# Optimization experiments

Hardware: AMD Instinct MI355X
Metric: run time of the kernel (lower is better)

## Reference

```python
import jax, jax.numpy as jnp
import numpy as np

STRIDES = (8, 16, 32)
IMG = 1024
CENTER_RADIUS = 2.5
N_CAND = 10  # SimOTA candidate top-k


def setup_inputs() -> dict:
    key = jax.random.key(0)
    ks = jax.random.split(key, 6)
    B, G = 16, 100
    sizes = [IMG // s for s in STRIDES]
    inp = {}
    for i, H in enumerate(sizes):
        inp[f"reg{i}"] = jax.random.normal(ks[i], (B, 4, H, H), jnp.float32)
        inp[f"obj{i}"] = jax.random.normal(ks[3 + i], (B, 1, H, H), jnp.float32)
    rng = np.random.default_rng(0)
    cxy = rng.uniform(64.0, IMG - 64.0, (B, G, 2))
    wh = rng.uniform(16.0, 160.0, (B, G, 2))
    labels = np.concatenate([np.zeros((B, G, 1)), cxy, wh], axis=-1).astype(np.float32)
    counts = rng.integers(20, G + 1, B)  # variable num_gt per image, zero-padded tail
    mask = (np.arange(G)[None, :] < counts[:, None]).astype(np.float32)
    labels = labels * mask[:, :, None]
    inp["labels"] = jnp.asarray(labels)
    return inp


def _decode(regs, objs):
    outs, xs, ys, ss = [], [], [], []
    for reg, obj, s in zip(regs, objs, STRIDES):
        B, _, H, W = reg.shape
        o = jnp.concatenate([reg, obj], axis=1).transpose(0, 2, 3, 1).reshape(B, H * W, 5)
        yv, xv = jnp.meshgrid(jnp.arange(H), jnp.arange(W), indexing="ij")
        grid = jnp.stack([xv, yv], axis=-1).reshape(-1, 2).astype(o.dtype)  # [HW,2] (x,y)
        xy = (o[..., :2] + grid) * s
        wh = jnp.exp(o[..., 2:4]) * s
        outs.append(jnp.concatenate([xy, wh, o[..., 4:5]], axis=-1))
        xs.append(grid[:, 0])
        ys.append(grid[:, 1])
        ss.append(jnp.full((H * W,), float(s), o.dtype))
    return (jnp.concatenate(outs, 1), jnp.concatenate(xs), jnp.concatenate(ys), jnp.concatenate(ss))


def _pairwise_iou(gt, pr):
    # gt [G,4], pr [A,4] in cxcywh -> [G,A]
    tl = jnp.maximum(gt[:, None, :2] - gt[:, None, 2:] * 0.5, pr[None, :, :2] - pr[None, :, 2:] * 0.5)
    br = jnp.minimum(gt[:, None, :2] + gt[:, None, 2:] * 0.5, pr[None, :, :2] + pr[None, :, 2:] * 0.5)
    en = jnp.all(tl < br, axis=-1)
    area_i = jnp.prod(br - tl, axis=-1) * en
    area_g = gt[:, 2] * gt[:, 3]
    area_p = pr[:, 2] * pr[:, 3]
    return area_i / (area_g[:, None] + area_p[None, :] - area_i + 1e-16)


def _iou_loss(pred, tgt):
    # elementwise cxcywh IoU loss: 1 - iou**2 (loss_type='iou')
    tl = jnp.maximum(pred[..., :2] - pred[..., 2:] * 0.5, tgt[..., :2] - tgt[..., 2:] * 0.5)
    br = jnp.minimum(pred[..., :2] + pred[..., 2:] * 0.5, tgt[..., :2] + tgt[..., 2:] * 0.5)
    en = jnp.all(tl < br, axis=-1)
    area_i = jnp.prod(br - tl, axis=-1) * en
    area_p = pred[..., 2] * pred[..., 3]
    area_g = tgt[..., 2] * tgt[..., 3]
    iou = area_i / (area_p + area_g - area_i + 1e-16)
    return 1.0 - iou ** 2


def _assign(gt_boxes, gt_valid, bbox, obj_logit, x_c, y_c, strides):
    # SimOTA assignment for one image. gt_boxes [G,4], bbox [A,4].
    G = gt_boxes.shape[0]
    gx, gy, gw, gh = gt_boxes[:, 0], gt_boxes[:, 1], gt_boxes[:, 2], gt_boxes[:, 3]
    bl = x_c[None] - (gx - 0.5 * gw)[:, None]
    br_ = (gx + 0.5 * gw)[:, None] - x_c[None]
    bt = y_c[None] - (gy - 0.5 * gh)[:, None]
    bb = (gy + 0.5 * gh)[:, None] - y_c[None]
    in_boxes = jnp.minimum(jnp.minimum(bl, br_), jnp.minimum(bt, bb)) > 0
    r = CENTER_RADIUS * strides[None]
    cl = x_c[None] - (gx[:, None] - r)
    cr = (gx[:, None] + r) - x_c[None]
    ct = y_c[None] - (gy[:, None] - r)
    cb = (gy[:, None] + r) - y_c[None]
    in_centers = jnp.minimum(jnp.minimum(cl, cr), jnp.minimum(ct, cb)) > 0
    fg_anchor = jnp.any(in_boxes, 0) | jnp.any(in_centers, 0)
    in_both = in_boxes & in_centers

    ious = _pairwise_iou(gt_boxes, bbox)                       # [G,A]
    valid_pair = gt_valid[:, None] & fg_anchor[None, :]
    ious_m = jnp.where(valid_pair, ious, 0.0)
    obj_cost = jax.nn.softplus(-obj_logit)[None, :]            # BCE-with-logits, target=1
    cost = (obj_cost + 3.0 * (-jnp.log(ious + 1e-8))
            + 1e5 * (~in_both) + 1e7 * (~valid_pair))

    topk_ious = jax.lax.top_k(ious_m, N_CAND)[0]               # [G,10]
    dyn_k = jnp.maximum(topk_ious.sum(1).astype(jnp.int32), 1)  # dynamic k per gt
    ranks = jnp.argsort(jnp.argsort(cost, axis=1), axis=1)      # rank of each anchor per gt
    matching = (ranks < dyn_k[:, None]) & gt_valid[:, None]
    n_match = matching.sum(0)
    best_gt = jnp.argmin(cost, axis=0)                          # conflict resolution
    resolved = (jnp.arange(G)[:, None] == best_gt[None, :]) & gt_valid[:, None]
    matching = jnp.where(n_match[None, :] > 1, resolved, matching)
    fg = jnp.any(matching, 0)
    matched_gt = jnp.argmax(matching, 0)
    return fg, matched_gt, fg.sum()


def reference(reg0, reg1, reg2, obj0, obj1, obj2, labels):
    out, x_sh, y_sh, strides = _decode((reg0, reg1, reg2), (obj0, obj1, obj2))
    bbox = out[..., :4]          # [B,A,4] decoded cxcywh
    obj_logit = out[..., 4]      # [B,A]
    x_c = (x_sh + 0.5) * strides
    y_c = (y_sh + 0.5) * strides
    gt_boxes = labels[..., 1:5]
    gt_valid = labels.sum(-1) > 0
    fg, matched_gt, nfg = jax.vmap(_assign, in_axes=(0, 0, 0, 0, None, None, None))(
        gt_boxes, gt_valid, bbox, obj_logit, x_c, y_c, strides)
    num_fg = jnp.maximum(nfg.sum().astype(jnp.float32), 1.0)
    reg_tgt = jax.vmap(lambda g, i: g[i])(gt_boxes, matched_gt)  # [B,A,4]
    fgf = fg.astype(jnp.float32)
    loss_iou = (_iou_loss(bbox, reg_tgt) * fgf).sum() / num_fg
    bce = jax.nn.softplus(obj_logit) - obj_logit * fgf           # BCEWithLogits
    loss_obj = bce.sum() / num_fg
    num_gts = jnp.maximum(gt_valid.sum().astype(jnp.float32), 1.0)
    loss = 5.0 * loss_iou + loss_obj
    return (loss, 5.0 * loss_iou, loss_obj, jnp.float32(0.0), num_fg / num_gts)
```

## Files before the change

### kernel.cpp

```cpp
#include <hip/hip_runtime.h>
#include <math.h>

#define NA   21504
#define NA0  16384
#define NA01 20480
#define NG   100
#define NB   16
#define NC   10
#define NCHK 84
#define NBLK 1344
#define MAXC 192
#define MCAP 1024
#define MSTRIDE 64
#define NSQ  4

__device__ __forceinline__ float softplusf(float x) {
    return fmaxf(x, 0.f) + log1pf(expf(-fabsf(x)));
}

__device__ __forceinline__ unsigned int fmono(float f) {
    unsigned int u = __float_as_uint(f);
    return (f < 0.f) ? ~u : (u | 0x80000000u);
}

__global__ __launch_bounds__(256) void k_decode(
    const float* __restrict__ reg0, const float* __restrict__ obj0,
    const float* __restrict__ reg1, const float* __restrict__ obj1,
    const float* __restrict__ reg2, const float* __restrict__ obj2,
    const float* __restrict__ labels,
    float4* __restrict__ A0, float* __restrict__ OC,
    int* __restrict__ cidx, int* __restrict__ bcnt,
    float* __restrict__ pSp)
{
    int b  = blockIdx.y;
    int bx = blockIdx.x;
    int tid = threadIdx.x;
    int a = bx * 256 + tid;

    int W, ry0, rows; float s;
    if (bx < 64)      { W = 128; s = 8.f;  ry0 = bx * 2;        rows = 2; }
    else if (bx < 80) { W = 64;  s = 16.f; ry0 = (bx - 64) * 4; rows = 4; }
    else              { W = 32;  s = 32.f; ry0 = (bx - 80) * 8; rows = 8; }

    __shared__ unsigned int smask[8];
    if (tid < 8) smask[tid] = 0u;
    __syncthreads();

    if (tid < NG) {
        const float* L = labels + (b * NG + tid) * 5;
        float gx = L[1], gy = L[2], gw = L[3], gh = L[4];
        float r = 2.5f * s;
        float tlx = gx - 0.5f * gw, tly = gy - 0.5f * gh;
        float brx = gx + 0.5f * gw, bry = gy + 0.5f * gh;
        float cxl = gx - r, cxh = gx + r, cyl = gy - r, cyh = gy + r;
        float lox = fminf(tlx, cxl), hix = fmaxf(brx, cxh);
        float loy = fminf(tly, cyl), hiy = fmaxf(bry, cyh);
        int ixA = (int)floorf(lox / s - 0.5f) - 1;
        int ixB = (int)ceilf (hix / s - 0.5f) + 1;
        int iyA = (int)floorf(loy / s - 0.5f) - 1;
        int iyB = (int)ceilf (hiy / s - 0.5f) + 1;
        ixA = max(ixA, 0); ixB = min(ixB, W - 1);
        iyA = max(iyA, ry0); iyB = min(iyB, ry0 + rows - 1);
        for (int iy = iyA; iy <= iyB; iy++) {
            float yc = ((float)iy + 0.5f) * s;
            float mb = fminf(yc - tly, bry - yc);
            float mc = fminf(yc - cyl, cyh - yc);
            for (int ix = ixA; ix <= ixB; ix++) {
                float xc = ((float)ix + 0.5f) * s;
                bool inb = fminf(fminf(xc - tlx, brx - xc), mb) > 0.f;
                bool inc = fminf(fminf(xc - cxl, cxh - xc), mc) > 0.f;
                if (inb || inc) {
                    int bit = (iy - ry0) * W + ix;
                    atomicOr(&smask[bit >> 5], 1u << (bit & 31));
                }
            }
        }
    }

    int x, y, hw, loc;
    const float* regp; const float* objp;
    if (a < NA0)       { x = a & 127;           y = a >> 7; hw = 16384; loc = y * 128 + x; regp = reg0; objp = obj0; }
    else if (a < NA01) { int i = a - NA0;  x = i & 63; y = i >> 6; hw = 4096;  loc = y * 64 + x;  regp = reg1; objp = obj1; }
    else               { int i = a - NA01; x = i & 31; y = i >> 5; hw = 1024;  loc = y * 32 + x;  regp = reg2; objp = obj2; }

    float r0 = regp[(b * 4 + 0) * hw + loc];
    float r1 = regp[(b * 4 + 1) * hw + loc];
    float r2 = regp[(b * 4 + 2) * hw + loc];
    float r3 = regp[(b * 4 + 3) * hw + loc];
    float ol = objp[b * hw + loc];

    float px = (r0 + (float)x) * s, py = (r1 + (float)y) * s;
    float pw = expf(r2) * s,        ph = expf(r3) * s;
    float ocv = softplusf(-ol);

    __syncthreads();
    bool fga = (smask[tid >> 5] >> (tid & 31)) & 1u;

    int idx = b * NA + a;
    if (fga) {
        A0[idx] = make_float4(px - 0.5f * pw, py - 0.5f * ph, px + 0.5f * pw, py + 0.5f * ph);
        OC[idx] = ocv;
    }

    float sp = ocv + ol;
    for (int off = 32; off > 0; off >>= 1) sp += __shfl_down(sp, off);

    unsigned long long mask = __ballot(fga);
    int lane = tid & 63, wid = tid >> 6;
    __shared__ float wSp[4];
    __shared__ int   wcnt[4];
    if (lane == 0) { wSp[wid] = sp; wcnt[wid] = __popcll(mask); }
    __syncthreads();
    int wbase = 0;
    #pragma unroll
    for (int w2 = 0; w2 < 4; w2++) if (w2 < wid) wbase += wcnt[w2];
    if (fga) {
        int prefix = __popcll(mask & ((1ull << lane) - 1ull));
        cidx[b * NA + bx * 256 + wbase + prefix] = a;
    }
    if (tid == 0) {
        bcnt[b * NCHK + bx] = wcnt[0] + wcnt[1] + wcnt[2] + wcnt[3];
        pSp[b * NCHK + bx]  = wSp[0] + wSp[1] + wSp[2] + wSp[3];
    }
}

__global__ __launch_bounds__(256) void k_pack(
    const float4* __restrict__ A0, const float* __restrict__ OC,
    const int* __restrict__ cidx, const int* __restrict__ bcnt,
    float4* __restrict__ PK0, float* __restrict__ PKO, int* __restrict__ PKA,
    int* __restrict__ fcnt,
    int* __restrict__ n_match, int* __restrict__ mg_min,
    unsigned long long* __restrict__ bestkey,
    int* __restrict__ mcount, int* __restrict__ fbflag)
{
    int b = blockIdx.y, bx = blockIdx.x, tid = threadIdx.x;
    int v = 0;
    for (int i = tid; i < bx; i += 256) v += bcnt[b * NCHK + i];
    for (int off = 32; off > 0; off >>= 1) v += __shfl_down(v, off);
    __shared__ int ws[4];
    int wid = tid >> 6;
    if ((tid & 63) == 0) ws[wid] = v;
    __syncthreads();
    int base = ws[0] + ws[1] + ws[2] + ws[3];
    int nt = bcnt[b * NCHK + bx];
    if (tid < nt) {
        int a = cidx[b * NA + bx * 256 + tid];
        int idx = b * NA + a;
        int d = b * NA + base + tid;
        PK0[d] = A0[idx];
        PKO[d] = OC[idx];
        PKA[d] = a;
        n_match[idx] = 0;
        mg_min[idx]  = 0x7fffffff;
        bestkey[idx] = 0xFFFFFFFFFFFFFFFFull;
    }
    if (bx == NCHK - 1 && tid == 0) fcnt[b] = base + nt;
    if (bx == 0 && tid == 0) { mcount[b * MSTRIDE] = 0; fbflag[b] = 0; }
}

__global__ __launch_bounds__(256) void k_assign(
    const float* __restrict__ labels, const float4* __restrict__ A0,
    const float* __restrict__ OC,
    const float4* __restrict__ PK0, const float* __restrict__ PKO,
    const int* __restrict__ PKA, const int* __restrict__ fcnt,
    int* __restrict__ n_match, int* __restrict__ mg_min,
    int* __restrict__ mlist, int* __restrict__ mcount,
    unsigned long long* __restrict__ bestkey, int* __restrict__ fbflag)
{
    int blk = blockIdx.x;
    int b = blk / NG, g = blk % NG;
    const float* L = labels + (b * NG + g) * 5;
    float l0 = L[0], gx = L[1], gy = L[2], gw = L[3], gh = L[4];
    bool gv = (l0 + gx + gy + gw + gh) > 0.f;
    if (!gv) return;
    int tid = threadIdx.x;

    float g_tlx = gx - 0.5f * gw, g_tly = gy - 0.5f * gh;
    float g_brx = gx + 0.5f * gw, g_bry = gy + 0.5f * gh;
    float ag = gw * gh;
    int bbase = b * NA;

    __shared__ float sio[256 * NC];
    __shared__ int   si2[256 * NC];
    __shared__ int   cand_a[MAXC];
    __shared__ float cand_c[MAXC];
    __shared__ int   scnt;
    if (tid == 0) scnt = 0;
    __syncthreads();

    int cnt = fcnt[b];

    float tio[NC];
    #pragma unroll
    for (int k = 0; k < NC; k++) tio[k] = 0.f;

    for (int m = tid; m < cnt; m += 256) {
        float4 c0 = PK0[bbase + m];
        float tlx = fmaxf(g_tlx, c0.x), tly = fmaxf(g_tly, c0.y);
        float brx = fminf(g_brx, c0.z), bry = fminf(g_bry, c0.w);
        if (tlx < brx && tly < bry) {
            float ai = (brx - tlx) * (bry - tly);
            float pa = (c0.z - c0.x) * (c0.w - c0.y);
            float iou = ai / (ag + pa - ai + 1e-16f);
            if (iou > tio[NC - 1]) {
                tio[NC - 1] = iou;
                #pragma unroll
                for (int j = NC - 1; j > 0; --j) {
                    if (tio[j] > tio[j - 1]) { float t = tio[j]; tio[j] = tio[j - 1]; tio[j - 1] = t; }
                }
            }
        }
    }

    #pragma unroll
    for (int k = 0; k < NC; k++) sio[tid * NC + k] = tio[k];
    __syncthreads();

    for (int off = 128; off > 0; off >>= 1) {
        if (tid < off) {
            int abase = tid * NC, bb2 = (tid + off) * NC;
            int i = 0, j = 0;
            float oo_[NC];
            #pragma unroll
            for (int k = 0; k < NC; k++) {
                float va = sio[abase + i], vb = sio[bb2 + j];
                bool ta = va >= vb;
                oo_[k] = ta ? va : vb;
                i += ta ? 1 : 0; j += ta ? 0 : 1;
            }
            #pragma unroll
            for (int k = 0; k < NC; k++) sio[abase + k] = oo_[k];
        }
        __syncthreads();
    }

    float s10 = 0.f;
    #pragma unroll
    for (int k = 0; k < NC; k++) s10 += sio[k];
    int dk = (int)s10;
    if (dk < 1) dk = 1;
    if (dk > NC) dk = NC;

    for (int lev = 0; lev < 3; lev++) {
        float s  = (lev == 0) ? 8.f : ((lev == 1) ? 16.f : 32.f);
        int   W  = (lev == 0) ? 128 : ((lev == 1) ? 64 : 32);
        int aofs = (lev == 0) ? 0 : ((lev == 1) ? NA0 : NA01);
        float rr = 2.5f * s;
        float gxr_lo = gx - rr, gxr_hi = gx + rr;
        float gyr_lo = gy - rr, gyr_hi = gy + rr;
        float lox = fmaxf(g_tlx, gxr_lo), hix = fminf(g_brx, gxr_hi);
        float loy = fmaxf(g_tly, gyr_lo), hiy = fminf(g_bry, gyr_hi);
        int ixA = (int)floorf(lox / s - 0.5f) - 1;
        int ixB = (int)ceilf (hix / s - 0.5f) + 1;
        int iyA = (int)floorf(loy / s - 0.5f) - 1;
        int iyB = (int)ceilf (hiy / s - 0.5f) + 1;
        ixA = max(ixA, 0); ixB = min(ixB, W - 1);
        iyA = max(iyA, 0); iyB = min(iyB, W - 1);
        int nx = ixB - ixA + 1, ny = iyB - iyA + 1;
        int nt = (nx > 0 && ny > 0) ? nx * ny : 0;
        for (int t = tid; t < nt; t += 256) {
            int ix = ixA + t % nx, iy = iyA + t / nx;
            float xcA = ((float)ix + 0.5f) * s;
            float ycA = ((float)iy + 0.5f) * s;
            float bl = xcA - g_tlx, brr = g_brx - xcA;
            float bt = ycA - g_tly, bbb = g_bry - ycA;
            bool inb = fminf(fminf(bl, brr), fminf(bt, bbb)) > 0.f;
            float cl = xcA - gxr_lo, cr = gxr_hi - xcA;
            float ct = ycA - gyr_lo, cb = gyr_hi - ycA;
            bool inc = fminf(fminf(cl, cr), fminf(ct, cb)) > 0.f;
            if (inb && inc) {
                int p = atomicAdd(&scnt, 1);
                if (p < MAXC) cand_a[p] = aofs + iy * W + ix;
            }
        }
    }
    __syncthreads();
    int nc_ = min(scnt, MAXC);

    if (dk <= nc_) {
        for (int ci = tid; ci < nc_; ci += 256) {
            int a = cand_a[ci];
            float4 c0 = A0[bbase + a];
            float pa = (c0.z - c0.x) * (c0.w - c0.y);
            float tlx = fmaxf(g_tlx, c0.x), tly = fmaxf(g_tly, c0.y);
            float brx = fminf(g_brx, c0.z), bry = fminf(g_bry, c0.w);
            bool en = (tlx < brx) && (tly < bry);
            float ai = en ? (brx - tlx) * (bry - tly) : 0.f;
            float iou = ai / (ag + pa - ai + 1e-16f);
            float c = OC[bbase + a] + 3.0f * (-__logf(iou + 1e-8f));
            cand_c[ci] = c;
            unsigned long long key = ((unsigned long long)fmono(c) << 32) | (unsigned int)g;
            atomicMin(&bestkey[bbase + a], key);
        }
        __syncthreads();
        for (int ci = tid; ci < nc_; ci += 256) {
            float c = cand_c[ci]; int a = cand_a[ci];
            int rank = 0;
            for (int j = 0; j < nc_; j++) {
                float cj = cand_c[j]; int aj = cand_a[j];
                rank += (cj < c || (cj == c && aj < a)) ? 1 : 0;
            }
            if (rank < dk) {
                if (atomicAdd(&n_match[bbase + a], 1) == 0) {
                    int p = atomicAdd(&mcount[b * MSTRIDE], 1);
                    mlist[b * MCAP + p] = a;
                }
                atomicMin(&mg_min[bbase + a], g);
            }
        }
    } else {
        if (tid == 0) fbflag[b] = 1;
        float fc[NC]; int fa[NC];
        #pragma unroll
        for (int k = 0; k < NC; k++) { fc[k] = 3.4e38f; fa[k] = 0x7fffffff; }
        for (int m = tid; m < cnt; m += 256) {
            int a = PKA[bbase + m];
            float4 c0 = PK0[bbase + m];
            float pa = (c0.z - c0.x) * (c0.w - c0.y);
            float tlx = fmaxf(g_tlx, c0.x), tly = fmaxf(g_tly, c0.y);
            float brx = fminf(g_brx, c0.z), bry = fminf(g_bry, c0.w);
            bool en = (tlx < brx) && (tly < bry);
            float ai = en ? (brx - tlx) * (bry - tly) : 0.f;
            float iou = ai / (ag + pa - ai + 1e-16f);
            int xx, yy; float s2;
            if (a < NA0)       { xx = a & 127;           yy = a >> 7;  s2 = 8.f;  }
            else if (a < NA01) { int i2 = a - NA0;  xx = i2 & 63; yy = i2 >> 6; s2 = 16.f; }
            else               { int i2 = a - NA01; xx = i2 & 31; yy = i2 >> 5; s2 = 32.f; }
            float xcA = ((float)xx + 0.5f) * s2, ycA = ((float)yy + 0.5f) * s2;
            float rr2 = 2.5f * s2;
            float bl = xcA - g_tlx, brr = g_brx - xcA;
            float bt = ycA - g_tly, bbb = g_bry - ycA;
            bool inb = fminf(fminf(bl, brr), fminf(bt, bbb)) > 0.f;
            float cl = xcA - (gx - rr2), cr = (gx + rr2) - xcA;
            float ct = ycA - (gy - rr2), cb = (gy + rr2) - ycA;
            bool inc = fminf(fminf(cl, cr), fminf(ct, cb)) > 0.f;
            float c = PKO[bbase + m] + 3.0f * (-__logf(iou + 1e-8f));
            if (!(inb && inc)) c += 100000.0f;
            if (c < fc[NC - 1] || (c == fc[NC - 1] && a < fa[NC - 1])) {
                fc[NC - 1] = c; fa[NC - 1] = a;
                #pragma unroll
                for (int j = NC - 1; j > 0; --j) {
                    bool sw = (fc[j] < fc[j - 1]) || (fc[j] == fc[j - 1] && fa[j] < fa[j - 1]);
                    if (sw) {
                        float t1 = fc[j]; fc[j] = fc[j - 1]; fc[j - 1] = t1;
                        int   t2 = fa[j]; fa[j] = fa[j - 1]; fa[j - 1] = t2;
                    }
                }
            }
        }
        __syncthreads();
        #pragma unroll
        for (int k = 0; k < NC; k++) { sio[tid * NC + k] = fc[k]; si2[tid * NC + k] = fa[k]; }
        __syncthreads();
        for (int off = 128; off > 0; off >>= 1) {
            if (tid < off) {
                int abase = tid * NC, bb2 = (tid + off) * NC;
                int i = 0, j = 0;
                float oc_[NC]; int oi_[NC];
                #pragma unroll
                for (int k = 0; k < NC; k++) {
                    float ca = sio[abase + i], cb3 = sio[bb2 + j];
                    int   ia = si2[abase + i], ib  = si2[bb2 + j];
                    bool ta = (ca < cb3) || (ca == cb3 && ia <= ib);
                    oc_[k] = ta ? ca : cb3; oi_[k] = ta ? ia : ib;
                    i += ta ? 1 : 0; j += ta ? 0 : 1;
                }
                #pragma unroll
                for (int k = 0; k < NC; k++) { sio[abase + k] = oc_[k]; si2[abase + k] = oi_[k]; }
            }
            __syncthreads();
        }
        if (tid == 0) {
            for (int k = 0; k < dk; k++) {
                int aa = si2[k];
                if (aa != 0x7fffffff) {
                    if (atomicAdd(&n_match[bbase + aa], 1) == 0) {
                        int p = atomicAdd(&mcount[b * MSTRIDE], 1);
                        mlist[b * MCAP + p] = aa;
                    }
                    atomicMin(&mg_min[bbase + aa], g);
                }
            }
        }
    }
}

__global__ __launch_bounds__(256) void k_sparse(
    const float* __restrict__ labels,
    const float* __restrict__ obj0, const float* __restrict__ obj1,
    const float* __restrict__ obj2,
    const float4* __restrict__ A0, const float* __restrict__ OC,
    const int* __restrict__ n_match, const int* __restrict__ mg_min,
    const int* __restrict__ mlist, const int* __restrict__ mcount,
    const unsigned long long* __restrict__ bestkey, const int* __restrict__ fbflag,
    float* __restrict__ pIl2, float* __restrict__ pOl, int* __restrict__ pNf2)
{
    int q = blockIdx.x;
    int b = blockIdx.y;
    int tid = threadIdx.x;
    __shared__ float lbl[NG * 5];
    for (int i = tid; i < NG * 5; i += 256) lbl[i] = labels[b * NG * 5 + i];
    __syncthreads();

    int cm = min(mcount[b * MSTRIDE], MCAP);
    int fb = fbflag[b];
    float il_s = 0.f, ol_s = 0.f; int nf = 0;

    for (int m = q * 256 + tid; m < cm; m += NSQ * 256) {
        int a = mlist[b * MCAP + m];
        int idx = b * NA + a;
        int n = n_match[idx];

        int x, y, hw, loc; const float* objp; float s, rr;
        if (a < NA0)       { x = a & 127;            y = a >> 7;  hw = 16384; loc = y * 128 + x; objp = obj0; s = 8.f;  rr = 20.f; }
        else if (a < NA01) { int i2 = a - NA0;  x = i2 & 63; y = i2 >> 6; hw = 4096; loc = y * 64 + x; objp = obj1; s = 16.f; rr = 40.f; }
        else               { int i2 = a - NA01; x = i2 & 31; y = i2 >> 5; hw = 1024; loc = y * 32 + x; objp = obj2; s = 32.f; rr = 80.f; }

        float4 c0 = A0[idx];
        bool fg = false; int mg = 0;
        if (n == 1) { fg = true; mg = mg_min[idx]; }
        else {
            unsigned long long key = fb ? 0xFFFFFFFFFFFFFFFFull : bestkey[idx];
            if (key != 0xFFFFFFFFFFFFFFFFull) {
                fg = true; mg = (int)(key & 0xFFFFFFFFull);
            } else {
                float pa = (c0.z - c0.x) * (c0.w - c0.y);
                float oc = OC[idx];
                float xcA = ((float)x + 0.5f) * s, ycA = ((float)y + 0.5f) * s;
                float bestc = 3.4e38f; int bg = 0;
                for (int g = 0; g < NG; g++) {
                    float l0 = lbl[g * 5 + 0], gx = lbl[g * 5 + 1], gy = lbl[g * 5 + 2];
                    float gw = lbl[g * 5 + 3], gh = lbl[g * 5 + 4];
                    bool gvv = (l0 + gx + gy + gw + gh) > 0.f;
                    float tlx = fmaxf(gx - 0.5f * gw, c0.x), tly = fmaxf(gy - 0.5f * gh, c0.y);
                    float brx = fminf(gx + 0.5f * gw, c0.z), bry = fminf(gy + 0.5f * gh, c0.w);
                    bool en = (tlx < brx) && (tly < bry);
                    float ai = en ? (brx - tlx) * (bry - tly) : 0.f;
                    float iou = ai / (gw * gh + pa - ai + 1e-16f);
                    float bl = xcA - (gx - 0.5f * gw), br = (gx + 0.5f * gw) - xcA;
                    float bt = ycA - (gy - 0.5f * gh), bb = (gy + 0.5f * gh) - ycA;
                    bool inb = fminf(fminf(bl, br), fminf(bt, bb)) > 0.f;
                    float cl = xcA - (gx - rr), cr = (gx + rr) - xcA;
                    float ct = ycA - (gy - rr), cb = (gy + rr) - ycA;
                    bool inc = fminf(fminf(cl, cr), fminf(ct, cb)) > 0.f;
                    float c = oc + 3.0f * (-__logf(iou + 1e-8f));
                    if (!(inb && inc)) c += 100000.0f;
                    if (!gvv)          c += 10000000.0f;
                    if (c < bestc) { bestc = c; bg = g; }
                }
                bool gvv = (lbl[bg * 5 + 0] + lbl[bg * 5 + 1] + lbl[bg * 5 + 2] +
                            lbl[bg * 5 + 3] + lbl[bg * 5 + 4]) > 0.f;
                if (gvv) { fg = true; mg = bg; }
            }
        }

        if (fg) {
            float pa = (c0.z - c0.x) * (c0.w - c0.y);
            float gx = lbl[mg * 5 + 1], gy = lbl[mg * 5 + 2];
            float gw = lbl[mg * 5 + 3], gh = lbl[mg * 5 + 4];
            float tlx = fmaxf(c0.x, gx - 0.5f * gw);
            float tly = fmaxf(c0.y, gy - 0.5f * gh);
            float brx = fminf(c0.z, gx + 0.5f * gw);
            float bry = fminf(c0.w, gy + 0.5f * gh);
            bool en = (tlx < brx) && (tly < bry);
            float ai = en ? (brx - tlx) * (bry - tly) : 0.f;
            float iou = ai / (pa + gw * gh - ai + 1e-16f);
            il_s += 1.f - iou * iou;
            ol_s += objp[b * hw + loc];
            nf++;
        }
    }

    for (int off = 32; off > 0; off >>= 1) {
        il_s += __shfl_down(il_s, off);
        ol_s += __shfl_down(ol_s, off);
        nf   += __shfl_down(nf, off);
    }
    __shared__ float wI[4], wO[4];
    __shared__ int   wN[4];
    int wid = tid >> 6;
    if ((tid & 63) == 0) { wI[wid] = il_s; wO[wid] = ol_s; wN[wid] = nf; }
    __syncthreads();
    if (tid == 0) {
        int pb = b * NSQ + q;
        pIl2[pb] = wI[0] + wI[1] + wI[2] + wI[3];
        pOl[pb]  = wO[0] + wO[1] + wO[2] + wO[3];
        pNf2[pb] = wN[0] + wN[1] + wN[2] + wN[3];
    }
}

__global__ __launch_bounds__(256) void k_fin(
    const float* __restrict__ pSp, const float* __restrict__ pIl2,
    const float* __restrict__ pOl, const int* __restrict__ pNf2,
    const float* __restrict__ labels, float* __restrict__ out)
{
    int tid = threadIdx.x;
    double dSp = 0.0;
    for (int i = tid; i < NBLK; i += 256) dSp += (double)pSp[i];
    double dIl = 0.0, dOl = 0.0; int nf = 0;
    for (int i = tid; i < NB * NSQ; i += 256) {
        dIl += (double)pIl2[i];
        dOl += (double)pOl[i];
        nf  += pNf2[i];
    }
    int ng = 0;
    for (int i = tid; i < NB * NG; i += 256) {
        const float* L = labels + i * 5;
        if (L[0] + L[1] + L[2] + L[3] + L[4] > 0.f) ng++;
    }
    for (int off = 32; off > 0; off >>= 1) {
        dSp += __shfl_down(dSp, off);
        dIl += __shfl_down(dIl, off);
        dOl += __shfl_down(dOl, off);
        nf  += __shfl_down(nf, off);
        ng  += __shfl_down(ng, off);
    }
    __shared__ double sSp[4], sIl[4], sOl[4];
    __shared__ int sNf[4], sNg[4];
    int wid = tid >> 6;
    if ((tid & 63) == 0) { sSp[wid] = dSp; sIl[wid] = dIl; sOl[wid] = dOl; sNf[wid] = nf; sNg[wid] = ng; }
    __syncthreads();
    if (tid == 0) {
        double tSp = sSp[0] + sSp[1] + sSp[2] + sSp[3];
        double tIl = sIl[0] + sIl[1] + sIl[2] + sIl[3];
        double tOl = sOl[0] + sOl[1] + sOl[2] + sOl[3];
        int tNf = sNf[0] + sNf[1] + sNf[2] + sNf[3];
        int tNg = sNg[0] + sNg[1] + sNg[2] + sNg[3];
        float num_fg  = fmaxf((float)tNf, 1.f);
        float num_gts = fmaxf((float)tNg, 1.f);
        float li = (float)(tIl / (double)num_fg);
        float lo = (float)((tSp - tOl) / (double)num_fg);
        out[0] = 5.f * li + lo;
        out[1] = 5.f * li;
        out[2] = lo;
        out[3] = 0.f;
        out[4] = num_fg / num_gts;
    }
}

extern "C" void kernel_launch(void* const* d_in, const int* in_sizes, int n_in,
                              void* d_out, int out_size, void* d_ws, size_t ws_size,
                              hipStream_t stream)
{
    const float* reg0   = (const float*)d_in[0];
    const float* obj0   = (const float*)d_in[1];
    const float* reg1   = (const float*)d_in[2];
    const float* obj1   = (const float*)d_in[3];
    const float* reg2   = (const float*)d_in[4];
    const float* obj2   = (const float*)d_in[5];
    const float* labels = (const float*)d_in[6];
    float* out = (float*)d_out;

    char* w = (char*)d_ws;
    size_t off = 0;
    int*    mcount = (int*)(w + off);     off += (size_t)NB * MSTRIDE * 4;
    int*    bcnt   = (int*)(w + off);     off += (size_t)NB * NCHK * 4;
    int*    fcnt   = (int*)(w + off);     off += (size_t)NB * 4;
    int*    fbflag = (int*)(w + off);     off += (size_t)NB * 4;
    float*  pSp    = (float*)(w + off);   off += (size_t)NBLK * 4;
    float*  pIl2   = (float*)(w + off);   off += (size_t)NB * NSQ * 4;
    float*  pOl    = (float*)(w + off);   off += (size_t)NB * NSQ * 4;
    int*    pNf2   = (int*)(w + off);     off += (size_t)NB * NSQ * 4;
    off = (off + 255) & ~(size_t)255;
    float4* A0      = (float4*)(w + off); off += (size_t)NB * NA * 16;
    float4* PK0     = (float4*)(w + off); off += (size_t)NB * NA * 16;
    unsigned long long* bestkey = (unsigned long long*)(w + off); off += (size_t)NB * NA * 8;
    float*  OC      = (float*)(w + off);  off += (size_t)NB * NA * 4;
    float*  PKO     = (float*)(w + off);  off += (size_t)NB * NA * 4;
    int*    PKA     = (int*)(w + off);    off += (size_t)NB * NA * 4;
    int*    cidx    = (int*)(w + off);    off += (size_t)NB * NA * 4;
    int*    n_match = (int*)(w + off);    off += (size_t)NB * NA * 4;
    int*    mg_min  = (int*)(w + off);    off += (size_t)NB * NA * 4;
    int*    mlist   = (int*)(w + off);    off += (size_t)NB * MCAP * 4;

    dim3 gA(NCHK, NB);

    k_decode<<<gA, 256, 0, stream>>>(reg0, obj0, reg1, obj1, reg2, obj2, labels,
                                     A0, OC, cidx, bcnt, pSp);
    k_pack<<<gA, 256, 0, stream>>>(A0, OC, cidx, bcnt, PK0, PKO, PKA, fcnt,
                                   n_match, mg_min, bestkey, mcount, fbflag);
    k_assign<<<dim3(NB * NG), 256, 0, stream>>>(labels, A0, OC, PK0, PKO, PKA, fcnt,
                                                n_match, mg_min, mlist, mcount,
                                                bestkey, fbflag);
    k_sparse<<<dim3(NSQ, NB), 256, 0, stream>>>(labels, obj0, obj1, obj2, A0, OC,
                                                n_match, mg_min, mlist, mcount,
                                                bestkey, fbflag, pIl2, pOl, pNf2);
    k_fin<<<1, 256, 0, stream>>>(pSp, pIl2, pOl, pNf2, labels, out);
}
```

Measured before the change: 122.0 us.

## Fuse pack into decode via atomic compaction and finalize in last sparse block

Result: no change. 123.4 us (+1.2%).

```diff
diff --git a/kernel.cpp b/kernel.cpp
--- a/kernel.cpp
+++ b/kernel.cpp
@@ -11,7 +11,7 @@
 #define NBLK 1344
 #define MAXC 192
 #define MCAP 1024
-#define MSTRIDE 64
+#define CSTRIDE 64
 #define NSQ  4
 
 __device__ __forceinline__ float softplusf(float x) {
@@ -29,7 +29,10 @@
     const float* __restrict__ reg2, const float* __restrict__ obj2,
     const float* __restrict__ labels,
     float4* __restrict__ A0, float* __restrict__ OC,
-    int* __restrict__ cidx, int* __restrict__ bcnt,
+    float4* __restrict__ PK0, float* __restrict__ PKO, int* __restrict__ PKA,
+    int* __restrict__ fcnt,
+    int* __restrict__ n_match, int* __restrict__ mg_min,
+    unsigned long long* __restrict__ bestkey,
     float* __restrict__ pSp)
 {
     int b  = blockIdx.y;
@@ -43,6 +46,9 @@
     else              { W = 32;  s = 32.f; ry0 = (bx - 80) * 8; rows = 8; }
 
     __shared__ unsigned int smask[8];
+    __shared__ float wSp[4];
+    __shared__ int   wcnt[4];
+    __shared__ int   sbase;
     if (tid < 8) smask[tid] = 0u;
     __syncthreads();
 
@@ -95,67 +101,41 @@
 
     __syncthreads();
     bool fga = (smask[tid >> 5] >> (tid & 31)) & 1u;
+    float4 corners = make_float4(px - 0.5f * pw, py - 0.5f * ph,
+                                 px + 0.5f * pw, py + 0.5f * ph);
 
     int idx = b * NA + a;
     if (fga) {
-        A0[idx] = make_float4(px - 0.5f * pw, py - 0.5f * ph, px + 0.5f * pw, py + 0.5f * ph);
+        A0[idx] = corners;
         OC[idx] = ocv;
-    }
-
-    float sp = ocv + ol;
-    for (int off = 32; off > 0; off >>= 1) sp += __shfl_down(sp, off);
-
-    unsigned long long mask = __ballot(fga);
-    int lane = tid & 63, wid = tid >> 6;
-    __shared__ float wSp[4];
-    __shared__ int   wcnt[4];
-    if (lane == 0) { wSp[wid] = sp; wcnt[wid] = __popcll(mask); }
-    __syncthreads();
-    int wbase = 0;
-    #pragma unroll
-    for (int w2 = 0; w2 < 4; w2++) if (w2 < wid) wbase += wcnt[w2];
-    if (fga) {
-        int prefix = __popcll(mask & ((1ull << lane) - 1ull));
-        cidx[b * NA + bx * 256 + wbase + prefix] = a;
-    }
-    if (tid == 0) {
-        bcnt[b * NCHK + bx] = wcnt[0] + wcnt[1] + wcnt[2] + wcnt[3];
-        pSp[b * NCHK + bx]  = wSp[0] + wSp[1] + wSp[2] + wSp[3];
-    }
-}
-
-__global__ __launch_bounds__(256) void k_pack(
-    const float4* __restrict__ A0, const float* __restrict__ OC,
-    const int* __restrict__ cidx, const int* __restrict__ bcnt,
-    float4* __restrict__ PK0, float* __restrict__ PKO, int* __restrict__ PKA,
-    int* __restrict__ fcnt,
-    int* __restrict__ n_match, int* __restrict__ mg_min,
-    unsigned long long* __restrict__ bestkey,
-    int* __restrict__ mcount, int* __restrict__ fbflag)
-{
-    int b = blockIdx.y, bx = blockIdx.x, tid = threadIdx.x;
-    int v = 0;
-    for (int i = tid; i < bx; i += 256) v += bcnt[b * NCHK + i];
-    for (int off = 32; off > 0; off >>= 1) v += __shfl_down(v, off);
-    __shared__ int ws[4];
-    int wid = tid >> 6;
-    if ((tid & 63) == 0) ws[wid] = v;
-    __syncthreads();
-    int base = ws[0] + ws[1] + ws[2] + ws[3];
-    int nt = bcnt[b * NCHK + bx];
-    if (tid < nt) {
-        int a = cidx[b * NA + bx * 256 + tid];
-        int idx = b * NA + a;
-        int d = b * NA + base + tid;
-        PK0[d] = A0[idx];
-        PKO[d] = OC[idx];
-        PKA[d] = a;
         n_match[idx] = 0;
         mg_min[idx]  = 0x7fffffff;
         bestkey[idx] = 0xFFFFFFFFFFFFFFFFull;
     }
-    if (bx == NCHK - 1 && tid == 0) fcnt[b] = base + nt;
-    if (bx == 0 && tid == 0) { mcount[b * MSTRIDE] = 0; fbflag[b] = 0; }
+
+    float sp = ocv + ol;
+    for (int off = 32; off > 0; off >>= 1) sp += __shfl_down(sp, off);
+
+    unsigned long long mask = __ballot(fga);
+    int lane = tid & 63, wid = tid >> 6;
+    if (lane == 0) { wSp[wid] = sp; wcnt[wid] = __popcll(mask); }
+    __syncthreads();
+    int btotal = wcnt[0] + wcnt[1] + wcnt[2] + wcnt[3];
+    if (tid == 0) {
+        sbase = atomicAdd(&fcnt[b * CSTRIDE], btotal);
+        pSp[b * NCHK + bx] = wSp[0] + wSp[1] + wSp[2] + wSp[3];
+    }
+    __syncthreads();
+    if (fga) {
+        int wbase = 0;
+        #pragma unroll
+        for (int w2 = 0; w2 < 4; w2++) if (w2 < wid) wbase += wcnt[w2];
+        int prefix = __popcll(mask & ((1ull << lane) - 1ull));
+        int d = b * NA + sbase + wbase + prefix;
+        PK0[d] = corners;
+        PKO[d] = ocv;
+        PKA[d] = a;
+    }
 }
 
 __global__ __launch_bounds__(256) void k_assign(
@@ -188,7 +168,7 @@
     if (tid == 0) scnt = 0;
     __syncthreads();
 
-    int cnt = fcnt[b];
+    int cnt = fcnt[b * CSTRIDE];
 
     float tio[NC];
     #pragma unroll
@@ -302,7 +282,7 @@
             }
             if (rank < dk) {
                 if (atomicAdd(&n_match[bbase + a], 1) == 0) {
-                    int p = atomicAdd(&mcount[b * MSTRIDE], 1);
+                    int p = atomicAdd(&mcount[b * CSTRIDE], 1);
                     mlist[b * MCAP + p] = a;
                 }
                 atomicMin(&mg_min[bbase + a], g);
@@ -375,7 +355,7 @@
                 int aa = si2[k];
                 if (aa != 0x7fffffff) {
                     if (atomicAdd(&n_match[bbase + aa], 1) == 0) {
-                        int p = atomicAdd(&mcount[b * MSTRIDE], 1);
+                        int p = atomicAdd(&mcount[b * CSTRIDE], 1);
                         mlist[b * MCAP + p] = aa;
                     }
                     atomicMin(&mg_min[bbase + aa], g);
@@ -393,16 +373,21 @@
     const int* __restrict__ n_match, const int* __restrict__ mg_min,
     const int* __restrict__ mlist, const int* __restrict__ mcount,
     const unsigned long long* __restrict__ bestkey, const int* __restrict__ fbflag,
-    float* __restrict__ pIl2, float* __restrict__ pOl, int* __restrict__ pNf2)
+    const float* __restrict__ pSp,
+    float* __restrict__ pIl2, float* __restrict__ pOl, int* __restrict__ pNf2,
+    int* __restrict__ gdone, float* __restrict__ out)
 {
     int q = blockIdx.x;
     int b = blockIdx.y;
     int tid = threadIdx.x;
     __shared__ float lbl[NG * 5];
+    __shared__ float wI[4], wO[4];
+    __shared__ int   wN[4];
+    __shared__ int   s_g;
     for (int i = tid; i < NG * 5; i += 256) lbl[i] = labels[b * NG * 5 + i];
     __syncthreads();
 
-    int cm = min(mcount[b * MSTRIDE], MCAP);
+    int cm = min(mcount[b * CSTRIDE], MCAP);
     int fb = fbflag[b];
     float il_s = 0.f, ol_s = 0.f; int nf = 0;
 
@@ -476,8 +461,6 @@
         ol_s += __shfl_down(ol_s, off);
         nf   += __shfl_down(nf, off);
     }
-    __shared__ float wI[4], wO[4];
-    __shared__ int   wN[4];
     int wid = tid >> 6;
     if ((tid & 63) == 0) { wI[wid] = il_s; wO[wid] = ol_s; wN[wid] = nf; }
     __syncthreads();
@@ -486,55 +469,53 @@
         pIl2[pb] = wI[0] + wI[1] + wI[2] + wI[3];
         pOl[pb]  = wO[0] + wO[1] + wO[2] + wO[3];
         pNf2[pb] = wN[0] + wN[1] + wN[2] + wN[3];
-    }
-}
-
-__global__ __launch_bounds__(256) void k_fin(
-    const float* __restrict__ pSp, const float* __restrict__ pIl2,
-    const float* __restrict__ pOl, const int* __restrict__ pNf2,
-    const float* __restrict__ labels, float* __restrict__ out)
-{
-    int tid = threadIdx.x;
-    double dSp = 0.0;
-    for (int i = tid; i < NBLK; i += 256) dSp += (double)pSp[i];
-    double dIl = 0.0, dOl = 0.0; int nf = 0;
-    for (int i = tid; i < NB * NSQ; i += 256) {
-        dIl += (double)pIl2[i];
-        dOl += (double)pOl[i];
-        nf  += pNf2[i];
-    }
-    int ng = 0;
-    for (int i = tid; i < NB * NG; i += 256) {
-        const float* L = labels + i * 5;
-        if (L[0] + L[1] + L[2] + L[3] + L[4] > 0.f) ng++;
-    }
-    for (int off = 32; off > 0; off >>= 1) {
-        dSp += __shfl_down(dSp, off);
-        dIl += __shfl_down(dIl, off);
-        dOl += __shfl_down(dOl, off);
-        nf  += __shfl_down(nf, off);
-        ng  += __shfl_down(ng, off);
-    }
-    __shared__ double sSp[4], sIl[4], sOl[4];
-    __shared__ int sNf[4], sNg[4];
-    int wid = tid >> 6;
-    if ((tid & 63) == 0) { sSp[wid] = dSp; sIl[wid] = dIl; sOl[wid] = dOl; sNf[wid] = nf; sNg[wid] = ng; }
-    __syncthreads();
-    if (tid == 0) {
-        double tSp = sSp[0] + sSp[1] + sSp[2] + sSp[3];
-        double tIl = sIl[0] + sIl[1] + sIl[2] + sIl[3];
-        double tOl = sOl[0] + sOl[1] + sOl[2] + sOl[3];
-        int tNf = sNf[0] + sNf[1] + sNf[2] + sNf[3];
-        int tNg = sNg[0] + sNg[1] + sNg[2] + sNg[3];
-        float num_fg  = fmaxf((float)tNf, 1.f);
-        float num_gts = fmaxf((float)tNg, 1.f);
-        float li = (float)(tIl / (double)num_fg);
-        float lo = (float)((tSp - tOl) / (double)num_fg);
-        out[0] = 5.f * li + lo;
-        out[1] = 5.f * li;
-        out[2] = lo;
-        out[3] = 0.f;
-        out[4] = num_fg / num_gts;
+        __threadfence();
+        s_g = atomicAdd(gdone, 1);
+    }
+    __syncthreads();
+
+    if (s_g == NSQ * NB - 1) {
+        __threadfence();
+        double dSp = 0.0;
+        for (int i = tid; i < NBLK; i += 256) dSp += (double)pSp[i];
+        double dIl = 0.0, dOl = 0.0; int nf2 = 0;
+        if (tid < NB * NSQ) {
+            dIl = (double)pIl2[tid];
+            dOl = (double)pOl[tid];
+            nf2 = pNf2[tid];
+        }
+        int ng = 0;
+        for (int i = tid; i < NB * NG; i += 256) {
+            const float* L2 = labels + i * 5;
+            if (L2[0] + L2[1] + L2[2] + L2[3] + L2[4] > 0.f) ng++;
+        }
+        for (int off = 32; off > 0; off >>= 1) {
+            dSp += __shfl_down(dSp, off);
+            dIl += __shfl_down(dIl, off);
+            dOl += __shfl_down(dOl, off);
+            nf2 += __shfl_down(nf2, off);
+            ng  += __shfl_down(ng, off);
+        }
+        __shared__ double fSp[4], fIl[4], fOl[4];
+        __shared__ int fNf[4], fNg[4];
+        if ((tid & 63) == 0) { fSp[wid] = dSp; fIl[wid] = dIl; fOl[wid] = dOl; fNf[wid] = nf2; fNg[wid] = ng; }
+        __syncthreads();
+        if (tid == 0) {
+            double tSp = fSp[0] + fSp[1] + fSp[2] + fSp[3];
+            double tIl = fIl[0] + fIl[1] + fIl[2] + fIl[3];
+            double tOl = fOl[0] + fOl[1] + fOl[2] + fOl[3];
+            int tNf = fNf[0] + fNf[1] + fNf[2] + fNf[3];
+            int tNg = fNg[0] + fNg[1] + fNg[2] + fNg[3];
+            float num_fg  = fmaxf((float)tNf, 1.f);
+            float num_gts = fmaxf((float)tNg, 1.f);
+            float li = (float)(tIl / (double)num_fg);
+            float lo = (float)((tSp - tOl) / (double)num_fg);
+            out[0] = 5.f * li + lo;
+            out[1] = 5.f * li;
+            out[2] = lo;
+            out[3] = 0.f;
+            out[4] = num_fg / num_gts;
+        }
     }
 }
 
@@ -553,10 +534,11 @@
 
     char* w = (char*)d_ws;
     size_t off = 0;
-    int*    mcount = (int*)(w + off);     off += (size_t)NB * MSTRIDE * 4;
-    int*    bcnt   = (int*)(w + off);     off += (size_t)NB * NCHK * 4;
-    int*    fcnt   = (int*)(w + off);     off += (size_t)NB * 4;
-    int*    fbflag = (int*)(w + off);     off += (size_t)NB * 4;
+    int*    fcnt   = (int*)(w + off);     off += (size_t)NB * CSTRIDE * 4;
+    int*    mcount = (int*)(w + off);     off += (size_t)NB * CSTRIDE * 4;
+    int*    fbflag = (int*)(w + off);     off += 256;
+    int*    gdone  = (int*)(w + off);     off += 256;
+    size_t zeroBytes = off;
     float*  pSp    = (float*)(w + off);   off += (size_t)NBLK * 4;
     float*  pIl2   = (float*)(w + off);   off += (size_t)NB * NSQ * 4;
     float*  pOl    = (float*)(w + off);   off += (size_t)NB * NSQ * 4;
@@ -568,22 +550,19 @@
     float*  OC      = (float*)(w + off);  off += (size_t)NB * NA * 4;
     float*  PKO     = (float*)(w + off);  off += (size_t)NB * NA * 4;
     int*    PKA     = (int*)(w + off);    off += (size_t)NB * NA * 4;
-    int*    cidx    = (int*)(w + off);    off += (size_t)NB * NA * 4;
     int*    n_match = (int*)(w + off);    off += (size_t)NB * NA * 4;
     int*    mg_min  = (int*)(w + off);    off += (size_t)NB * NA * 4;
     int*    mlist   = (int*)(w + off);    off += (size_t)NB * MCAP * 4;
 
-    dim3 gA(NCHK, NB);
-
-    k_decode<<<gA, 256, 0, stream>>>(reg0, obj0, reg1, obj1, reg2, obj2, labels,
-                                     A0, OC, cidx, bcnt, pSp);
-    k_pack<<<gA, 256, 0, stream>>>(A0, OC, cidx, bcnt, PK0, PKO, PKA, fcnt,
-                                   n_match, mg_min, bestkey, mcount, fbflag);
+    hipMemsetAsync(w, 0, zeroBytes, stream);
+    k_decode<<<dim3(NCHK, NB), 256, 0, stream>>>(reg0, obj0, reg1, obj1, reg2, obj2,
+                                                 labels, A0, OC, PK0, PKO, PKA, fcnt,
+                                                 n_match, mg_min, bestkey, pSp);
     k_assign<<<dim3(NB * NG), 256, 0, stream>>>(labels, A0, OC, PK0, PKO, PKA, fcnt,
                                                 n_match, mg_min, mlist, mcount,
                                                 bestkey, fbflag);
     k_sparse<<<dim3(NSQ, NB), 256, 0, stream>>>(labels, obj0, obj1, obj2, A0, OC,
                                                 n_match, mg_min, mlist, mcount,
-                                                bestkey, fbflag, pIl2, pOl, pNf2);
-    k_fin<<<1, 256, 0, stream>>>(pSp, pIl2, pOl, pNf2, labels, out);
+                                                bestkey, fbflag, pSp,
+                                                pIl2, pOl, pNf2, gdone, out);
 }
```
